# Kernel optimization log

Hardware: AMD Instinct MI355X
Metric: run time of the kernel (lower is better)

The kernel has to match this reference:

```python
import jax, jax.numpy as jnp
import numpy as np

T, B, N = 16, 32, 4096
NUM_TYPES = 20
F = NUM_TYPES + 5  # 4 geo feats + one-hot type + valid flag
H = 8              # poly_hidden_layers
HID = 128          # hidden_layers


def _w(k, i, o):
    return jax.random.normal(k, (i, o), jnp.float32) / np.sqrt(i)


def setup_inputs() -> dict:
    key = jax.random.key(0)
    ks = jax.random.split(key, 8)
    points = jax.random.normal(ks[0], (T, B, N, F), jnp.float32)
    return {
        "points": points,
        "W1": _w(ks[1], F, H), "b1": jnp.zeros((H,), jnp.float32),
        "W2": _w(ks[2], H, H), "b2": jnp.zeros((H,), jnp.float32),
        "W3": _w(ks[3], H, H), "b3": jnp.zeros((H,), jnp.float32),
        "W4": _w(ks[4], 2 * H, H), "b4": jnp.zeros((H,), jnp.float32),
        "W5": _w(ks[5], H, H), "b5": jnp.zeros((H,), jnp.float32),
        "W6": _w(ks[6], H, H), "b6": jnp.zeros((H,), jnp.float32),
        "Wout": _w(ks[7], NUM_TYPES * H, HID), "bout": jnp.zeros((HID,), jnp.float32),
    }


def reference(points, W1, b1, W2, b2, W3, b3, W4, b4, W5, b5, W6, b6, Wout, bout):
    t, b, n, f = points.shape
    nt = f - 5
    x = points.reshape(t * b * n, f)
    valid = (x[:, -1:] != 0)                      # (TBN,1) nonzero == True, as jnp.where on floats
    types = jnp.argmax(x[:, 4:-1], axis=1)        # (TBN,) polyline type per point

    h = jax.nn.relu(x @ W1 + b1)
    h = jax.nn.relu(h @ W2 + b2)
    h = jax.nn.relu(h @ W3 + b3)
    h = jnp.where(valid, h, 0.0)                  # zero-out invalid points

    # segment id = (t,b) slot * num_types + type; pooling is per (t,b,type)
    tb = jnp.arange(t * b * n) // n
    seg = tb * nt + types
    num_seg = t * b * nt
    # original masks non-matching points to 0 then takes max over N; since h >= 0
    # (relu + zero masking), that equals max(segment_max, 0); empty types -> 0.
    pooled = jnp.maximum(jax.ops.segment_max(h, seg, num_segments=num_seg), 0.0)

    h = jnp.concatenate([h, pooled[seg]], axis=-1)  # (TBN, 2H)
    h = jax.nn.relu(h @ W4 + b4)
    h = jax.nn.relu(h @ W5 + b5)
    h = jax.nn.relu(h @ W6 + b6)
    h = jnp.where(valid, h, 0.0)

    pooled2 = jnp.maximum(jax.ops.segment_max(h, seg, num_segments=num_seg), 0.0)
    out = pooled2.reshape(t, b, nt * h.shape[-1])   # types concatenated along feature dim
    return jax.nn.relu(out @ Wout + bout)           # (T, B, hidden_layers)
```

## Files before the change

### kernel.cpp

```cpp
#include <hip/hip_runtime.h>

#define T_ 16
#define B_ 32
#define N_ 4096
#define NT 20
#define F_ 25
#define H_ 8
#define HID_ 128
#define PSTR 9
#define SEGF_ (NT*H_)
#define BT 512
#define NSUB (N_/BT)
#define CF (BT*F_)

typedef __attribute__((address_space(1))) const void GV;
typedef __attribute__((address_space(3))) void LV;

__device__ __forceinline__ void g2l16(const float* g, float* l) {
  __builtin_amdgcn_global_load_lds((GV*)g, (LV*)l, 16, 0, 0);
}
__device__ __forceinline__ void g2l4(const float* g, float* l) {
  __builtin_amdgcn_global_load_lds((GV*)g, (LV*)l, 4, 0, 0);
}

__device__ __forceinline__ unsigned f2bf(float x) {
  unsigned u = __float_as_uint(x);
  u += 0x7fffu + ((u >> 16) & 1u);
  return u >> 16;
}
__device__ __forceinline__ float bf2f(unsigned s) { return __uint_as_float(s << 16); }

template<int NI>
__device__ __forceinline__ void layer(const float* in, const float* __restrict__ W,
                                      const float* __restrict__ b, float* out) {
#pragma unroll
  for (int j = 0; j < H_; j++) {
    float a = b[j];
#pragma unroll
    for (int f = 0; f < NI; f++) a = fmaf(in[f], W[f*H_ + j], a);
    out[j] = fmaxf(a, 0.0f);
  }
}

extern "C" __global__ __launch_bounds__(BT, 4)
void kFused(const float* __restrict__ pts,
            const float* __restrict__ W1, const float* __restrict__ b1,
            const float* __restrict__ W2, const float* __restrict__ b2,
            const float* __restrict__ W3, const float* __restrict__ b3,
            const float* __restrict__ W4, const float* __restrict__ b4,
            const float* __restrict__ W5, const float* __restrict__ b5,
            const float* __restrict__ W6, const float* __restrict__ b6,
            const float* __restrict__ Wout, const float* __restrict__ bout,
            float* __restrict__ out)
{
  __shared__ float xs[CF];
  __shared__ int lp1[NT*PSTR];
  __shared__ int lp2[NT*PSTR];
  const int tid = threadIdx.x;
  const int tb = blockIdx.x;
  if (tid < NT*PSTR) { lp1[tid] = 0; lp2[tid] = 0; }

  const float* base = pts + (size_t)tb * (N_*F_);

#define ISSUE(S)                                                         \
  {                                                                      \
    const float* gc = base + (S)*CF;                                     \
    _Pragma("unroll")                                                    \
    for (int k = 0; k < 6; k++)                                          \
      g2l16(gc + (tid + k*BT)*4, xs + (tid + k*BT)*4);                   \
    g2l4(gc + 6*4*BT + tid, xs + 6*4*BT + tid);                          \
  }

  uint4 h3p[NSUB];
  int   tyv[NSUB];

  ISSUE(0)

#define PH1(S)                                                           \
  {                                                                      \
    __syncthreads();    \
    float xv[F_];                                                        \
    _Pragma("unroll")                                                    \
    for (int f = 0; f < F_; f++) xv[f] = xs[tid*F_ + f];                 \
    __syncthreads();                  \
    if ((S) < NSUB-1) ISSUE((S)+1)                                       \
    int ty = 0; float best = xv[4];                                      \
    _Pragma("unroll")                                                    \
    for (int k = 1; k < NT; k++)                                         \
      if (xv[4+k] > best) { best = xv[4+k]; ty = k; }                    \
    const bool valid = (xv[F_-1] != 0.0f);                               \
    float t1[H_], t2[H_];                                                \
    layer<F_>(xv, W1, b1, t1);                                           \
    layer<H_>(t1, W2, b2, t2);                                           \
    layer<H_>(t2, W3, b3, t1);                                           \
    if (!valid) {                                                        \
      _Pragma("unroll")                                                  \
      for (int j = 0; j < H_; j++) t1[j] = 0.0f;                         \
    }                                                                    \
    h3p[S].x = f2bf(t1[0]) | (f2bf(t1[1]) << 16);                        \
    h3p[S].y = f2bf(t1[2]) | (f2bf(t1[3]) << 16);                        \
    h3p[S].z = f2bf(t1[4]) | (f2bf(t1[5]) << 16);                        \
    h3p[S].w = f2bf(t1[6]) | (f2bf(t1[7]) << 16);                        \
    tyv[S] = valid ? ty : -1;                                            \
    if (valid) {                                                         \
      _Pragma("unroll")                                                  \
      for (int j = 0; j < H_; j++)                                       \
        atomicMax(&lp1[ty*PSTR + j], __float_as_int(t1[j]));             \
    }                                                                    \
  }

  PH1(0) PH1(1) PH1(2) PH1(3) PH1(4) PH1(5) PH1(6) PH1(7)

  __syncthreads();

#define PH2(S)                                                           \
  {                                                                      \
    const int ty = tyv[S];                                               \
    if (ty >= 0) {                                                       \
      float x16[2*H_];                                                   \
      x16[0] = bf2f(h3p[S].x & 0xffffu); x16[1] = bf2f(h3p[S].x >> 16);  \
      x16[2] = bf2f(h3p[S].y & 0xffffu); x16[3] = bf2f(h3p[S].y >> 16);  \
      x16[4] = bf2f(h3p[S].z & 0xffffu); x16[5] = bf2f(h3p[S].z >> 16);  \
      x16[6] = bf2f(h3p[S].w & 0xffffu); x16[7] = bf2f(h3p[S].w >> 16);  \
      _Pragma("unroll")                                                  \
      for (int j = 0; j < H_; j++)                                       \
        x16[H_+j] = __int_as_float(lp1[ty*PSTR + j]);                    \
      float t1[H_], t2[H_];                                              \
      layer<2*H_>(x16, W4, b4, t1);                                      \
      layer<H_>(t1, W5, b5, t2);                                         \
      layer<H_>(t2, W6, b6, t1);                                         \
      _Pragma("unroll")                                                  \
      for (int j = 0; j < H_; j++)                                       \
        atomicMax(&lp2[ty*PSTR + j], __float_as_int(t1[j]));             \
    }                                                                    \
  }

  PH2(0) PH2(1) PH2(2) PH2(3) PH2(4) PH2(5) PH2(6) PH2(7)

  __syncthreads();

  if (tid < HID_) {
    float a = bout[tid];
#pragma unroll 4
    for (int k = 0; k < SEGF_; k++) {
      const float v = __int_as_float(lp2[(k >> 3)*PSTR + (k & 7)]);
      a = fmaf(v, Wout[k*HID_ + tid], a);
    }
    out[tb*HID_ + tid] = fmaxf(a, 0.0f);
  }
#undef ISSUE
#undef PH1
#undef PH2
}

extern "C" void kernel_launch(void* const* d_in, const int* in_sizes, int n_in,
                              void* d_out, int out_size, void* d_ws, size_t ws_size,
                              hipStream_t stream) {
  const float* pts  = (const float*)d_in[0];
  const float* W1   = (const float*)d_in[1];  const float* b1 = (const float*)d_in[2];
  const float* W2   = (const float*)d_in[3];  const float* b2 = (const float*)d_in[4];
  const float* W3   = (const float*)d_in[5];  const float* b3 = (const float*)d_in[6];
  const float* W4   = (const float*)d_in[7];  const float* b4 = (const float*)d_in[8];
  const float* W5   = (const float*)d_in[9];  const float* b5 = (const float*)d_in[10];
  const float* W6   = (const float*)d_in[11]; const float* b6 = (const float*)d_in[12];
  const float* Wout = (const float*)d_in[13]; const float* bout = (const float*)d_in[14];
  float* out = (float*)d_out;

  kFused<<<T_*B_, BT, 0, stream>>>(pts, W1, b1, W2, b2, W3, b3,
                                   W4, b4, W5, b5, W6, b6, Wout, bout, out);
}
```

Baseline: 67.13 us.

## Double-buffer LDS point chunks with two loads in flight and explicit vmcnt waits

Splits the LDS staging buffer into two halves so the next two chunks of points are prefetched while the current chunk is computed. Barriers become raw s_barrier calls guarded by explicit vmcnt/lgkmcnt waits so a chunk's loads are awaited while the following chunk's loads stay outstanding. This doubles the LDS footprint (about 100 KB per block), so launch bounds drop to 2 blocks per CU, trading occupancy for deeper memory prefetch.

```diff
diff --git a/kernel.cpp b/kernel.cpp
--- a/kernel.cpp
+++ b/kernel.cpp
@@ -42,7 +42,7 @@
   }
 }
 
-extern "C" __global__ __launch_bounds__(BT, 4)
+extern "C" __global__ __launch_bounds__(BT, 2)
 void kFused(const float* __restrict__ pts,
             const float* __restrict__ W1, const float* __restrict__ b1,
             const float* __restrict__ W2, const float* __restrict__ b2,
@@ -53,7 +53,7 @@
             const float* __restrict__ Wout, const float* __restrict__ bout,
             float* __restrict__ out)
 {
-  __shared__ float xs[CF];
+  __shared__ float xs[2][CF];
   __shared__ int lp1[NT*PSTR];
   __shared__ int lp2[NT*PSTR];
   const int tid = threadIdx.x;
@@ -62,28 +62,37 @@
 
   const float* base = pts + (size_t)tb * (N_*F_);
 
-#define ISSUE(S)                                                         \
+#define ISSUE(S, BUF)                                                    \
   {                                                                      \
     const float* gc = base + (S)*CF;                                     \
+    float* lb = xs[BUF];                                                 \
     _Pragma("unroll")                                                    \
     for (int k = 0; k < 6; k++)                                          \
-      g2l16(gc + (tid + k*BT)*4, xs + (tid + k*BT)*4);                   \
-    g2l4(gc + 6*4*BT + tid, xs + 6*4*BT + tid);                          \
+      g2l16(gc + (tid + k*BT)*4, lb + (tid + k*BT)*4);                   \
+    g2l4(gc + 6*4*BT + tid, lb + 6*4*BT + tid);                          \
   }
 
   uint4 h3p[NSUB];
   int   tyv[NSUB];
 
-  ISSUE(0)
+  ISSUE(0, 0)
+  ISSUE(1, 1)
 
-#define PH1(S)                                                           \
+#define PH1(S, WN, DOISS)                                                \
   {                                                                      \
-    __syncthreads();    \
+    asm volatile("s_waitcnt vmcnt(" #WN ")" ::: "memory");               \
+    __builtin_amdgcn_sched_barrier(0);                                   \
+    __builtin_amdgcn_s_barrier();          \
+    __builtin_amdgcn_sched_barrier(0);                                   \
     float xv[F_];                                                        \
+    const float* xb = xs[(S)&1];                                         \
     _Pragma("unroll")                                                    \
-    for (int f = 0; f < F_; f++) xv[f] = xs[tid*F_ + f];                 \
-    __syncthreads();                  \
-    if ((S) < NSUB-1) ISSUE((S)+1)                                       \
+    for (int f = 0; f < F_; f++) xv[f] = xb[tid*F_ + f];                 \
+    asm volatile("s_waitcnt lgkmcnt(0)" ::: "memory");                   \
+    __builtin_amdgcn_sched_barrier(0);                                   \
+    __builtin_amdgcn_s_barrier();          \
+    __builtin_amdgcn_sched_barrier(0);                                   \
+    if (DOISS) ISSUE((S)+2, (S)&1)                                       \
     int ty = 0; float best = xv[4];                                      \
     _Pragma("unroll")                                                    \
     for (int k = 1; k < NT; k++)                                         \
@@ -109,7 +118,8 @@
     }                                                                    \
   }
 
-  PH1(0) PH1(1) PH1(2) PH1(3) PH1(4) PH1(5) PH1(6) PH1(7)
+  PH1(0,7,1) PH1(1,7,1) PH1(2,7,1) PH1(3,7,1)
+  PH1(4,7,1) PH1(5,7,1) PH1(6,7,0) PH1(7,0,0)
 
   __syncthreads();
 
```

After: 95.63 us. 1.42x slower.

## Process two slots per block with per-wave triple-buffered async loads

Applied to the files above, without the earlier changes.

Each block now handles two (t,b) slots, halving the grid to 256 blocks. Each wave loads its own 64-point slice into a triple-buffered LDS ring and waits with per-wave vmcnt/lgkmcnt instead of block-wide __syncthreads. Loads for the second slot are issued while the first slot's phase-2 and output stages run. The aim is to hide global-load latency and remove barrier stalls, at the cost of fewer blocks (launch bounds lowered to 2), larger LDS use, and correctness that depends on the hand-placed waitcnt values.

```diff
diff --git a/kernel.cpp b/kernel.cpp
--- a/kernel.cpp
+++ b/kernel.cpp
@@ -10,8 +10,11 @@
 #define PSTR 9
 #define SEGF_ (NT*H_)
 #define BT 512
-#define NSUB (N_/BT)
+#define NW 8
+#define WPTS 64
+#define WFL (WPTS*F_)
 #define CF (BT*F_)
+#define NCHUNK 16
 
 typedef __attribute__((address_space(1))) const void GV;
 typedef __attribute__((address_space(3))) void LV;
@@ -42,7 +45,13 @@
   }
 }
 
-extern "C" __global__ __launch_bounds__(BT, 4)
+#define LBAR()                                                  \
+  { asm volatile("s_waitcnt lgkmcnt(0)" ::: "memory");          \
+    __builtin_amdgcn_sched_barrier(0);                          \
+    __builtin_amdgcn_s_barrier();                               \
+    __builtin_amdgcn_sched_barrier(0); }
+
+extern "C" __global__ __launch_bounds__(BT, 2)
 void kFused(const float* __restrict__ pts,
             const float* __restrict__ W1, const float* __restrict__ b1,
             const float* __restrict__ W2, const float* __restrict__ b2,
@@ -53,37 +62,44 @@
             const float* __restrict__ Wout, const float* __restrict__ bout,
             float* __restrict__ out)
 {
-  __shared__ float xs[CF];
+  __shared__ float xs[3][NW][WFL];
   __shared__ int lp1[NT*PSTR];
   __shared__ int lp2[NT*PSTR];
-  const int tid = threadIdx.x;
-  const int tb = blockIdx.x;
+  const int tid  = threadIdx.x;
+  const int wid  = tid >> 6;
+  const int lane = tid & 63;
   if (tid < NT*PSTR) { lp1[tid] = 0; lp2[tid] = 0; }
-
-  const float* base = pts + (size_t)tb * (N_*F_);
-
-#define ISSUE(S)                                                         \
+  __syncthreads();
+
+  const float* gblk = pts + (size_t)blockIdx.x * (2*N_*F_);
+
+#define ISSUE(C)                                                         \
   {                                                                      \
-    const float* gc = base + (S)*CF;                                     \
+    const float* gc = gblk + (size_t)(C)*CF + wid*WFL;                   \
+    float* lb = &xs[(C)%3][wid][0];                                      \
     _Pragma("unroll")                                                    \
     for (int k = 0; k < 6; k++)                                          \
-      g2l16(gc + (tid + k*BT)*4, xs + (tid + k*BT)*4);                   \
-    g2l4(gc + 6*4*BT + tid, xs + 6*4*BT + tid);                          \
-  }
-
-  uint4 h3p[NSUB];
-  int   tyv[NSUB];
+      g2l16(gc + k*256 + lane*4, lb + k*256 + lane*4);                   \
+    g2l4(gc + 1536 + lane, lb + 1536 + lane);                            \
+  }
+
+  uint4 h3p[NW];
+  int   tyv[NW];
 
   ISSUE(0)
-
-#define PH1(S)                                                           \
+  ISSUE(1)
+
+#define STEP(C, WN, DOISS)                                               \
   {                                                                      \
-    __syncthreads();    \
+    asm volatile("s_waitcnt vmcnt(" #WN ")" ::: "memory");               \
+    __builtin_amdgcn_sched_barrier(0);                                   \
     float xv[F_];                                                        \
+    const float* xb = &xs[(C)%3][wid][lane*F_];                          \
     _Pragma("unroll")                                                    \
-    for (int f = 0; f < F_; f++) xv[f] = xs[tid*F_ + f];                 \
-    __syncthreads();                  \
-    if ((S) < NSUB-1) ISSUE((S)+1)                                       \
+    for (int f = 0; f < F_; f++) xv[f] = xb[f];                          \
+    asm volatile("s_waitcnt lgkmcnt(0)" ::: "memory");                   \
+    __builtin_amdgcn_sched_barrier(0);                                   \
+    if (DOISS) ISSUE((C)+2)                                              \
     int ty = 0; float best = xv[4];                                      \
     _Pragma("unroll")                                                    \
     for (int k = 1; k < NT; k++)                                         \
@@ -97,21 +113,17 @@
       _Pragma("unroll")                                                  \
       for (int j = 0; j < H_; j++) t1[j] = 0.0f;                         \
     }                                                                    \
-    h3p[S].x = f2bf(t1[0]) | (f2bf(t1[1]) << 16);                        \
-    h3p[S].y = f2bf(t1[2]) | (f2bf(t1[3]) << 16);                        \
-    h3p[S].z = f2bf(t1[4]) | (f2bf(t1[5]) << 16);                        \
-    h3p[S].w = f2bf(t1[6]) | (f2bf(t1[7]) << 16);                        \
-    tyv[S] = valid ? ty : -1;                                            \
+    h3p[(C)&7].x = f2bf(t1[0]) | (f2bf(t1[1]) << 16);                    \
+    h3p[(C)&7].y = f2bf(t1[2]) | (f2bf(t1[3]) << 16);                    \
+    h3p[(C)&7].z = f2bf(t1[4]) | (f2bf(t1[5]) << 16);                    \
+    h3p[(C)&7].w = f2bf(t1[6]) | (f2bf(t1[7]) << 16);                    \
+    tyv[(C)&7] = valid ? ty : -1;                                        \
     if (valid) {                                                         \
       _Pragma("unroll")                                                  \
       for (int j = 0; j < H_; j++)                                       \
         atomicMax(&lp1[ty*PSTR + j], __float_as_int(t1[j]));             \
     }                                                                    \
   }
-
-  PH1(0) PH1(1) PH1(2) PH1(3) PH1(4) PH1(5) PH1(6) PH1(7)
-
-  __syncthreads();
 
 #define PH2(S)                                                           \
   {                                                                      \
@@ -135,22 +147,39 @@
     }                                                                    \
   }
 
+#define PH3(SLOT)                                                        \
+  if (tid < HID_) {                                                      \
+    float a = bout[tid];                                                 \
+    _Pragma("unroll 4")                                                  \
+    for (int k = 0; k < SEGF_; k++) {                                    \
+      const float v = __int_as_float(lp2[(k >> 3)*PSTR + (k & 7)]);      \
+      a = fmaf(v, Wout[k*HID_ + tid], a);                                \
+    }                                                                    \
+    out[((size_t)blockIdx.x*2 + (SLOT))*HID_ + tid] = fmaxf(a, 0.0f);    \
+  }
+
+  STEP(0,7,1) STEP(1,7,1) STEP(2,7,1) STEP(3,7,1)
+  STEP(4,7,1) STEP(5,7,1) STEP(6,7,1) STEP(7,7,1)
+  LBAR()
   PH2(0) PH2(1) PH2(2) PH2(3) PH2(4) PH2(5) PH2(6) PH2(7)
-
-  __syncthreads();
-
-  if (tid < HID_) {
-    float a = bout[tid];
-#pragma unroll 4
-    for (int k = 0; k < SEGF_; k++) {
-      const float v = __int_as_float(lp2[(k >> 3)*PSTR + (k & 7)]);
-      a = fmaf(v, Wout[k*HID_ + tid], a);
-    }
-    out[tb*HID_ + tid] = fmaxf(a, 0.0f);
-  }
+  LBAR()
+  PH3(0)
+  LBAR()
+  if (tid < NT*PSTR) { lp1[tid] = 0; lp2[tid] = 0; }
+  LBAR()
+
+  STEP(8,7,1)  STEP(9,7,1)  STEP(10,7,1) STEP(11,7,1)
+  STEP(12,7,1) STEP(13,7,1) STEP(14,7,0) STEP(15,0,0)
+  LBAR()
+  PH2(0) PH2(1) PH2(2) PH2(3) PH2(4) PH2(5) PH2(6) PH2(7)
+  LBAR()
+  PH3(1)
+
 #undef ISSUE
-#undef PH1
+#undef STEP
 #undef PH2
+#undef PH3
+#undef LBAR
 }
 
 extern "C" void kernel_launch(void* const* d_in, const int* in_sizes, int n_in,
@@ -166,6 +195,6 @@
   const float* Wout = (const float*)d_in[13]; const float* bout = (const float*)d_in[14];
   float* out = (float*)d_out;
 
-  kFused<<<T_*B_, BT, 0, stream>>>(pts, W1, b1, W2, b2, W3, b3,
-                                   W4, b4, W5, b5, W6, b6, Wout, bout, out);
-}
+  kFused<<<T_*B_/2, BT, 0, stream>>>(pts, W1, b1, W2, b2, W3, b3,
+                                     W4, b4, W5, b5, W6, b6, Wout, bout, out);
+}
```

Measured after the change: 88.75 us. 32.2% more time.
